# Kernel optimization log

Hardware: AMD Instinct MI355X
Metric: run time of the kernel (lower is better)

The kernel has to match this reference:

```python
import jax, jax.numpy as jnp
import numpy as np

HEADS = 8
DIM_HEAD = 64
QUERY_DIM = 512
CONTEXT_DIM = 512
OUT_DIM = 512
INNER = HEADS * DIM_HEAD  # 512


def setup_inputs() -> dict:
    key = jax.random.key(0)
    ks = jax.random.split(key, 6)
    B, N, S, M = 2, 1024, 4, 2048
    x = jax.random.normal(ks[0], (B, N, S, QUERY_DIM), dtype=jnp.float32)
    context = jax.random.normal(ks[1], (B, M, CONTEXT_DIM), dtype=jnp.float32)
    # Linear weights stored as [in, out] so y = x @ W (matches torch Linear with W.T)
    Wq = jax.random.normal(ks[2], (QUERY_DIM, INNER), dtype=jnp.float32) / np.sqrt(QUERY_DIM)
    Wkv = jax.random.normal(ks[3], (CONTEXT_DIM, 2 * INNER), dtype=jnp.float32) / np.sqrt(CONTEXT_DIM)
    Wo = jax.random.normal(ks[4], (INNER, OUT_DIM), dtype=jnp.float32) / np.sqrt(INNER)
    bo = jax.random.normal(ks[5], (OUT_DIM,), dtype=jnp.float32) * 0.01
    return {"x": x, "context": context, "Wq": Wq, "Wkv": Wkv, "Wo": Wo, "bo": bo}


def reference(x, context, Wq, Wkv, Wo, bo):
    B, N, S, _ = x.shape
    M = context.shape[1]
    scale = DIM_HEAD ** -0.5
    # projections
    q = (x @ Wq).reshape(B, N, S, HEADS, DIM_HEAD)            # b n s h d
    kv = context @ Wkv                                        # b m (2*inner)
    k, v = jnp.split(kv, 2, axis=-1)
    k = k.reshape(B, M, HEADS, DIM_HEAD)                      # b m h d
    v = v.reshape(B, M, HEADS, DIM_HEAD)
    # attention scores: [(b h) s n m] expressed as bhsnm
    sim = jnp.einsum('bnshd,bmhd->bhsnm', q, k) * scale
    attn = jax.nn.softmax(sim, axis=-1)
    out = jnp.einsum('bhsnm,bmhd->bnshd', attn, v)            # b n s h d
    out = out.reshape(B, N, S, INNER)
    return out @ Wo + bo
```

## Files before the change

### kernel.cpp

```cpp
#include <hip/hip_runtime.h>

typedef __bf16 bf16;
typedef __bf16 bf16x8 __attribute__((ext_vector_type(8)));
typedef __bf16 bf16x4 __attribute__((ext_vector_type(4)));
typedef float f32x4 __attribute__((ext_vector_type(4)));

#define SCL 0.18033688011112042f

#define GLOAD_LDS16(g, l)                                          \
  __builtin_amdgcn_global_load_lds(                                \
      (const __attribute__((address_space(1))) void*)(g),          \
      (__attribute__((address_space(3))) void*)(l), 16, 0, 0)

static __device__ __forceinline__ unsigned pk_bf16(float a, float b) {
  union { bf16 h[2]; unsigned u; } cv;
  cv.h[0] = (bf16)a; cv.h[1] = (bf16)b;
  return cv.u;
}
static __device__ __forceinline__ void pl32swap(unsigned& a, unsigned& b) {
  auto r = __builtin_amdgcn_permlane32_swap(a, b, false, false);
  a = r[0]; b = r[1];
}
static __device__ __forceinline__ void pl16swap(unsigned& a, unsigned& b) {
  auto r = __builtin_amdgcn_permlane16_swap(a, b, false, false);
  a = r[0]; b = r[1];
}

__global__ __launch_bounds__(256) void prep_kernel(const float* __restrict__ x,
                                                   const float* __restrict__ ctx,
                                                   const float* __restrict__ Wq,
                                                   const float* __restrict__ Wkv,
                                                   const float* __restrict__ Wo,
                                                   bf16* __restrict__ xb,
                                                   bf16* __restrict__ cb,
                                                   bf16* __restrict__ Wqt,
                                                   bf16* __restrict__ Wkvt,
                                                   bf16* __restrict__ Wot) {
  const int bid = blockIdx.x;
  const int tid = threadIdx.x;
  if (bid < 3072) {
    const float* src;
    bf16* dst;
    size_t off;
    if (bid < 2048) { src = x; dst = xb; off = (size_t)bid * 2048; }
    else            { src = ctx; dst = cb; off = (size_t)(bid - 2048) * 2048; }
    size_t i = off + (size_t)tid * 8;
    float4 a0 = *(const float4*)&src[i];
    float4 a1 = *(const float4*)&src[i + 4];
    bf16x8 o;
    o[0] = (bf16)a0.x; o[1] = (bf16)a0.y; o[2] = (bf16)a0.z; o[3] = (bf16)a0.w;
    o[4] = (bf16)a1.x; o[5] = (bf16)a1.y; o[6] = (bf16)a1.z; o[7] = (bf16)a1.w;
    *(bf16x8*)&dst[i] = o;
  } else {
    __shared__ float tile[32][33];
    const int idx = bid - 3072;
    const int bx = idx & 63;
    const int k0 = (idx >> 6) * 32;
    const float* W; bf16* Wt; int N, n0;
    if (bx < 16)      { W = Wq;  Wt = Wqt;  N = 512;  n0 = bx * 32; }
    else if (bx < 48) { W = Wkv; Wt = Wkvt; N = 1024; n0 = (bx - 16) * 32; }
    else              { W = Wo;  Wt = Wot;  N = 512;  n0 = (bx - 48) * 32; }
    const int j = tid & 31, i0 = tid >> 5;
#pragma unroll
    for (int ii = 0; ii < 4; ii++) {
      int i = i0 * 4 + ii;
      tile[i][j] = W[(size_t)(k0 + i) * N + n0 + j];
    }
    __syncthreads();
#pragma unroll
    for (int ii = 0; ii < 4; ii++) {
      int i = i0 * 4 + ii;
      Wt[(size_t)(n0 + i) * 512 + k0 + j] = (bf16)tile[j][i];
    }
  }
}

__device__ __forceinline__ void gemm128x64_core(const bf16* __restrict__ A,
                                                const bf16* __restrict__ Bt,
                                                int m0, int n0,
                                                bf16* As, bf16* Bs,
                                                f32x4 (&acc)[4][2],
                                                int wave, int lane) {
  const int l15 = lane & 15, quad = lane >> 4;
  const int psw = l15 & 7;
  const int lrow = lane >> 3;
  const int gchunk = (lane & 7) ^ lrow;
  const bf16* Ag = A + (size_t)(m0 + wave * 32 + lrow) * 512 + gchunk * 8;
  const bf16* Bg = Bt + (size_t)(n0 + wave * 16 + lrow) * 512 + gchunk * 8;
  bf16* Asw = As + wave * 32 * 64;
  bf16* Bsw = Bs + wave * 16 * 64;
  const int wm = (wave >> 1) * 64, wn = (wave & 1) * 32;

#pragma unroll
  for (int g = 0; g < 4; g++)
    GLOAD_LDS16(Ag + (size_t)(g * 8) * 512, Asw + g * 8 * 64);
#pragma unroll
  for (int g = 0; g < 2; g++)
    GLOAD_LDS16(Bg + (size_t)(g * 8) * 512, Bsw + g * 8 * 64);
  __syncthreads();

  for (int t = 0; t < 8; t++) {
    if (t < 7) {
      const int kt = (t + 1) * 64;
      const int nb = (t + 1) & 1;
#pragma unroll
      for (int g = 0; g < 4; g++)
        GLOAD_LDS16(Ag + kt + (size_t)(g * 8) * 512, Asw + nb * (128 * 64) + g * 8 * 64);
#pragma unroll
      for (int g = 0; g < 2; g++)
        GLOAD_LDS16(Bg + kt + (size_t)(g * 8) * 512, Bsw + nb * (64 * 64) + g * 8 * 64);
    }
    const bf16* Ac = As + (t & 1) * (128 * 64);
    const bf16* Bc = Bs + (t & 1) * (64 * 64);
#pragma unroll
    for (int h = 0; h < 2; h++) {
      bf16x8 af[4], bfr[2];
#pragma unroll
      for (int i = 0; i < 4; i++)
        af[i] = *(const bf16x8*)&Ac[(wm + i * 16 + l15) * 64 + (((h * 4 + quad) ^ psw) * 8)];
#pragma unroll
      for (int j = 0; j < 2; j++)
        bfr[j] = *(const bf16x8*)&Bc[(wn + j * 16 + l15) * 64 + (((h * 4 + quad) ^ psw) * 8)];
#pragma unroll
      for (int i = 0; i < 4; i++)
#pragma unroll
        for (int j = 0; j < 2; j++)
          acc[i][j] = __builtin_amdgcn_mfma_f32_16x16x32_bf16(af[i], bfr[j], acc[i][j], 0, 0, 0);
    }
    __syncthreads();
  }
}

__global__ __launch_bounds__(256, 2) void proj_kernel(const bf16* __restrict__ xb,
                                                      const bf16* __restrict__ cb,
                                                      const bf16* __restrict__ Wqt,
                                                      const bf16* __restrict__ Wkvt,
                                                      bf16* __restrict__ qb,
                                                      bf16* __restrict__ Kb,
                                                      bf16* __restrict__ Vtb) {
  __shared__ __align__(16) bf16 As[2 * 128 * 64];
  __shared__ __align__(16) bf16 Bs[2 * 64 * 64];
  const int tid = threadIdx.x;
  const int wave = tid >> 6, lane = tid & 63;
  const int quad = lane >> 4, l15 = lane & 15;
  const int bid = blockIdx.x;
  f32x4 acc[4][2] = {};
  const int wm = (wave >> 1) * 64, wn = (wave & 1) * 32;

  if (bid < 512) {
    const int m0 = (bid & 63) * 128, n0 = (bid >> 6) * 64;
    gemm128x64_core(xb, Wqt, m0, n0, As, Bs, acc, wave, lane);
#pragma unroll
    for (int i = 0; i < 4; i++) {
      const int rowb = m0 + wm + i * 16 + quad * 4;
#pragma unroll
      for (int j = 0; j < 2; j++) {
        const int col = n0 + wn + j * 16 + l15;
#pragma unroll
        for (int r = 0; r < 4; r++)
          qb[(size_t)(rowb + r) * 512 + col] = (bf16)(acc[i][j][r] * SCL);
      }
    }
  } else {
    const int idx = bid - 512;
    const int m0 = (idx & 31) * 128, n0 = (idx >> 5) * 64;
    gemm128x64_core(cb, Wkvt, m0, n0, As, Bs, acc, wave, lane);
#pragma unroll
    for (int i = 0; i < 4; i++) {
      const int rowb = m0 + wm + i * 16 + quad * 4;
#pragma unroll
      for (int j = 0; j < 2; j++) {
        const int col = n0 + wn + j * 16 + l15;
        if (col < 512) {
#pragma unroll
          for (int r = 0; r < 4; r++)
            Kb[(size_t)(rowb + r) * 512 + col] = (bf16)acc[i][j][r];
        } else {
          const int hh = (col - 512) >> 6, d = (col - 512) & 63;
          const int bb = rowb >> 11, mb = rowb & 2047;
          bf16x4 pk;
          pk[0] = (bf16)acc[i][j][0]; pk[1] = (bf16)acc[i][j][1];
          pk[2] = (bf16)acc[i][j][2]; pk[3] = (bf16)acc[i][j][3];
          *(bf16x4*)&Vtb[((size_t)(bb * 8 + hh) * 64 + d) * 2048 + mb] = pk;
        }
      }
    }
  }
}

__global__ __launch_bounds__(256, 2) void outproj_kernel(const bf16* __restrict__ attn,
                                                         const bf16* __restrict__ Wot,
                                                         float* __restrict__ out,
                                                         const float* __restrict__ bias) {
  __shared__ __align__(16) bf16 As[2 * 128 * 64];
  __shared__ __align__(16) bf16 Bs[2 * 64 * 64];
  const int tid = threadIdx.x;
  const int wave = tid >> 6, lane = tid & 63;
  const int quad = lane >> 4, l15 = lane & 15;
  const int bid = blockIdx.x;
  const int m0 = (bid & 63) * 128, n0 = (bid >> 6) * 64;
  f32x4 acc[4][2] = {};
  gemm128x64_core(attn, Wot, m0, n0, As, Bs, acc, wave, lane);
  const int wm = (wave >> 1) * 64, wn = (wave & 1) * 32;
#pragma unroll
  for (int i = 0; i < 4; i++) {
    const int rowb = m0 + wm + i * 16 + quad * 4;
#pragma unroll
    for (int j = 0; j < 2; j++) {
      const int col = n0 + wn + j * 16 + l15;
      const float bv = bias[col];
#pragma unroll
      for (int r = 0; r < 4; r++)
        out[(size_t)(rowb + r) * 512 + col] = acc[i][j][r] + bv;
    }
  }
}

__global__ __launch_bounds__(256, 2) void attn_kernel(const bf16* __restrict__ q,
                                                      const bf16* __restrict__ Kb,
                                                      const bf16* __restrict__ Vtb,
                                                      bf16* __restrict__ attn_out) {
  const int tid = threadIdx.x;
  const int wave = tid >> 6, lane = tid & 63;
  const int quad = lane >> 4, l15 = lane & 15;
  const int bid = blockIdx.x;
  const int g = bid & 15, inner = bid >> 4;
  const int b = g >> 3, h = g & 7;
  const int s = inner & 3, nt = inner >> 2;
  const int n0 = nt * 128;

  __shared__ __align__(16) bf16 Kl[2][64 * 64];
  __shared__ __align__(16) bf16 Vl[2][64 * 64];

  size_t qoff[2];
  bf16x8 qf[2][2];
#pragma unroll
  for (int cg = 0; cg < 2; cg++) {
    const int n = n0 + wave * 32 + cg * 16 + l15;
    qoff[cg] = ((size_t)((b * 1024 + n) * 4 + s)) * 512 + h * 64;
    qf[cg][0] = *(const bf16x8*)&q[qoff[cg] + quad * 8];
    qf[cg][1] = *(const bf16x8*)&q[qoff[cg] + 32 + quad * 8];
  }

  f32x4 o[2][4] = {};
  f32x4 ol[2] = {};
  bf16x8 ones;
#pragma unroll
  for (int i = 0; i < 8; i++) ones[i] = (bf16)1.0f;

  const int srow = tid >> 2, c0 = tid & 3;
  const bf16* Kg = Kb + (size_t)(b * 2048 + srow) * 512 + h * 64 + c0 * 16;
  const bf16* Vg = Vtb + ((size_t)(b * 8 + h) * 64 + srow) * 2048 + c0 * 16;
  const int ssw = srow & 7;
  const int koff0 = srow * 64 + ((c0 * 2) ^ ssw) * 8;
  const int koff1 = srow * 64 + ((c0 * 2 + 1) ^ ssw) * 8;

  uint4 kr0 = *(const uint4*)Kg;
  uint4 kr1 = *(const uint4*)(Kg + 8);
  uint4 vr0 = *(const uint4*)Vg;
  uint4 vr1 = *(const uint4*)(Vg + 8);
  *(uint4*)&Kl[0][koff0] = kr0; *(uint4*)&Kl[0][koff1] = kr1;
  *(uint4*)&Vl[0][koff0] = vr0; *(uint4*)&Vl[0][koff1] = vr1;

  const int psw = l15 & 7;

  for (int t = 0; t < 32; ++t) {
    __syncthreads();
    if (t < 31) {
      const bf16* kg = Kg + (size_t)(t + 1) * 64 * 512;
      const bf16* vg = Vg + (t + 1) * 64;
      kr0 = *(const uint4*)kg; kr1 = *(const uint4*)(kg + 8);
      vr0 = *(const uint4*)vg; vr1 = *(const uint4*)(vg + 8);
    }
    const bf16* Kc = &Kl[t & 1][0];
    const bf16* Vc = &Vl[t & 1][0];

    __builtin_amdgcn_s_setprio(1);

    f32x4 sf[2][4];
#pragma unroll
    for (int mc = 0; mc < 4; mc++) {
      bf16x8 kf0 = *(const bf16x8*)&Kc[(mc * 16 + l15) * 64 + ((quad ^ psw) * 8)];
      bf16x8 kf1 = *(const bf16x8*)&Kc[(mc * 16 + l15) * 64 + (((4 + quad) ^ psw) * 8)];
#pragma unroll
      for (int cg = 0; cg < 2; cg++) {
        f32x4 z = {};
        z = __builtin_amdgcn_mfma_f32_16x16x32_bf16(kf0, qf[cg][0], z, 0, 0, 0);
        z = __builtin_amdgcn_mfma_f32_16x16x32_bf16(kf1, qf[cg][1], z, 0, 0, 0);
        sf[cg][mc] = z;
      }
    }

    unsigned w[2][4][2];
#pragma unroll
    for (int cg = 0; cg < 2; cg++)
#pragma unroll
      for (int mc = 0; mc < 4; mc++) {
        const float e0 = __builtin_amdgcn_exp2f(sf[cg][mc][0]);
        const float e1 = __builtin_amdgcn_exp2f(sf[cg][mc][1]);
        const float e2 = __builtin_amdgcn_exp2f(sf[cg][mc][2]);
        const float e3 = __builtin_amdgcn_exp2f(sf[cg][mc][3]);
        w[cg][mc][0] = pk_bf16(e0, e1);
        w[cg][mc][1] = pk_bf16(e2, e3);
      }

    bf16x8 pf[2][2];
#pragma unroll
    for (int cg = 0; cg < 2; cg++)
#pragma unroll
      for (int mch = 0; mch < 2; mch++) {
        unsigned tw0, tw1, tw2, tw3;
        {
          unsigned a = w[cg][2 * mch][0], bb2 = w[cg][2 * mch + 1][0];
          pl32swap(a, bb2);
          pl16swap(a, bb2);
          tw0 = a; tw2 = bb2;
        }
        {
          unsigned a = w[cg][2 * mch][1], bb2 = w[cg][2 * mch + 1][1];
          pl32swap(a, bb2);
          pl16swap(a, bb2);
          tw1 = a; tw3 = bb2;
        }
        union { unsigned u[4]; bf16x8 v; } cv;
        cv.u[0] = tw0; cv.u[1] = tw1; cv.u[2] = tw2; cv.u[3] = tw3;
        pf[mch][cg] = cv.v;
      }

#pragma unroll
    for (int mch = 0; mch < 2; mch++) {
#pragma unroll
      for (int dg = 0; dg < 4; dg++) {
        bf16x8 vf = *(const bf16x8*)&Vc[(dg * 16 + l15) * 64 + (((mch * 4 + quad) ^ psw)) * 8];
#pragma unroll
        for (int cg = 0; cg < 2; cg++)
          o[cg][dg] = __builtin_amdgcn_mfma_f32_16x16x32_bf16(vf, pf[mch][cg], o[cg][dg], 0, 0, 0);
      }
#pragma unroll
      for (int cg = 0; cg < 2; cg++)
        ol[cg] = __builtin_amdgcn_mfma_f32_16x16x32_bf16(ones, pf[mch][cg], ol[cg], 0, 0, 0);
    }

    __builtin_amdgcn_s_setprio(0);

    if (t < 31) {
      bf16* Kn = &Kl[(t + 1) & 1][0];
      bf16* Vn = &Vl[(t + 1) & 1][0];
      *(uint4*)&Kn[koff0] = kr0; *(uint4*)&Kn[koff1] = kr1;
      *(uint4*)&Vn[koff0] = vr0; *(uint4*)&Vn[koff1] = vr1;
    }
  }

#pragma unroll
  for (int cg = 0; cg < 2; cg++) {
    const float inv = 1.0f / ol[cg][0];
#pragma unroll
    for (int dg = 0; dg < 4; dg++) {
      bf16x4 ok;
      ok[0] = (bf16)(o[cg][dg][0] * inv); ok[1] = (bf16)(o[cg][dg][1] * inv);
      ok[2] = (bf16)(o[cg][dg][2] * inv); ok[3] = (bf16)(o[cg][dg][3] * inv);
      *(bf16x4*)&attn_out[qoff[cg] + dg * 16 + quad * 4] = ok;
    }
  }
}

extern "C" void kernel_launch(void* const* d_in, const int* in_sizes, int n_in,
                              void* d_out, int out_size, void* d_ws, size_t ws_size,
                              hipStream_t stream) {
  const float* x = (const float*)d_in[0];
  const float* context = (const float*)d_in[1];
  const float* Wq = (const float*)d_in[2];
  const float* Wkv = (const float*)d_in[3];
  const float* Wo = (const float*)d_in[4];
  const float* bo = (const float*)d_in[5];
  float* out = (float*)d_out;

  char* ws = (char*)d_ws;
  bf16* xb   = (bf16*)(ws);
  bf16* cb   = (bf16*)(ws + (8u << 20));
  bf16* qb   = (bf16*)(ws + (12u << 20));
  bf16* Kb   = (bf16*)(ws + (20u << 20));
  bf16* Vtb  = (bf16*)(ws + (24u << 20));
  bf16* Wqt  = (bf16*)(ws + (28u << 20));
  bf16* Wkvt = (bf16*)(ws + (28u << 20) + 524288);
  bf16* Wot  = (bf16*)(ws + (28u << 20) + 1572864);
  bf16* attn = xb;

  prep_kernel<<<4096, 256, 0, stream>>>(x, context, Wq, Wkv, Wo, xb, cb, Wqt, Wkvt, Wot);
  proj_kernel<<<1024, 256, 0, stream>>>(xb, cb, Wqt, Wkvt, qb, Kb, Vtb);
  attn_kernel<<<512, 256, 0, stream>>>(qb, Kb, Vtb, attn);
  outproj_kernel<<<512, 256, 0, stream>>>(attn, Wot, out, bo);
}
```

Before: 151.3 us.

## Software-pipeline attention loop so QK of next tile overlaps PV of current

Restructures the flash-attention main loop into a skewed pipeline. Each iteration issues the QK^T MFMAs for tile t+1, then the PV MFMAs for tile t, then the exp/permute for t+1, with double-buffered P fragments. K is prefetched two tiles ahead and V one tile ahead. The aim is to hide the exp and permlane latency behind MFMA work, at the cost of more registers and more complex buffer indexing.

```diff
diff --git a/kernel.cpp b/kernel.cpp
--- a/kernel.cpp
+++ b/kernel.cpp
@@ -255,29 +255,13 @@
   const int koff0 = srow * 64 + ((c0 * 2) ^ ssw) * 8;
   const int koff1 = srow * 64 + ((c0 * 2 + 1) ^ ssw) * 8;
 
-  uint4 kr0 = *(const uint4*)Kg;
-  uint4 kr1 = *(const uint4*)(Kg + 8);
-  uint4 vr0 = *(const uint4*)Vg;
-  uint4 vr1 = *(const uint4*)(Vg + 8);
-  *(uint4*)&Kl[0][koff0] = kr0; *(uint4*)&Kl[0][koff1] = kr1;
-  *(uint4*)&Vl[0][koff0] = vr0; *(uint4*)&Vl[0][koff1] = vr1;
-
   const int psw = l15 & 7;
 
-  for (int t = 0; t < 32; ++t) {
-    __syncthreads();
-    if (t < 31) {
-      const bf16* kg = Kg + (size_t)(t + 1) * 64 * 512;
-      const bf16* vg = Vg + (t + 1) * 64;
-      kr0 = *(const uint4*)kg; kr1 = *(const uint4*)(kg + 8);
-      vr0 = *(const uint4*)vg; vr1 = *(const uint4*)(vg + 8);
-    }
-    const bf16* Kc = &Kl[t & 1][0];
-    const bf16* Vc = &Vl[t & 1][0];
-
-    __builtin_amdgcn_s_setprio(1);
-
-    f32x4 sf[2][4];
+  f32x4 sf[2][4];
+  bf16x8 pf_a[2][2], pf_b[2][2];
+  uint4 kr0, kr1, vr0, vr1;
+
+  auto qk_mfma = [&](const bf16* Kc) {
 #pragma unroll
     for (int mc = 0; mc < 4; mc++) {
       bf16x8 kf0 = *(const bf16x8*)&Kc[(mc * 16 + l15) * 64 + ((quad ^ psw) * 8)];
@@ -290,7 +274,9 @@
         sf[cg][mc] = z;
       }
     }
-
+  };
+
+  auto qk_finish = [&](bf16x8 (&pf)[2][2]) {
     unsigned w[2][4][2];
 #pragma unroll
     for (int cg = 0; cg < 2; cg++)
@@ -303,8 +289,6 @@
         w[cg][mc][0] = pk_bf16(e0, e1);
         w[cg][mc][1] = pk_bf16(e2, e3);
       }
-
-    bf16x8 pf[2][2];
 #pragma unroll
     for (int cg = 0; cg < 2; cg++)
 #pragma unroll
@@ -326,7 +310,9 @@
         cv.u[0] = tw0; cv.u[1] = tw1; cv.u[2] = tw2; cv.u[3] = tw3;
         pf[mch][cg] = cv.v;
       }
-
+  };
+
+  auto pv_step = [&](const bf16* Vc, const bf16x8 (&pf)[2][2]) {
 #pragma unroll
     for (int mch = 0; mch < 2; mch++) {
 #pragma unroll
@@ -340,15 +326,51 @@
       for (int cg = 0; cg < 2; cg++)
         ol[cg] = __builtin_amdgcn_mfma_f32_16x16x32_bf16(ones, pf[mch][cg], ol[cg], 0, 0, 0);
     }
-
+  };
+
+  kr0 = *(const uint4*)Kg;            kr1 = *(const uint4*)(Kg + 8);
+  vr0 = *(const uint4*)Vg;            vr1 = *(const uint4*)(Vg + 8);
+  *(uint4*)&Kl[0][koff0] = kr0; *(uint4*)&Kl[0][koff1] = kr1;
+  *(uint4*)&Vl[0][koff0] = vr0; *(uint4*)&Vl[0][koff1] = vr1;
+  kr0 = *(const uint4*)(Kg + 64 * 512);
+  kr1 = *(const uint4*)(Kg + 64 * 512 + 8);
+  __syncthreads();
+  qk_mfma(&Kl[0][0]);
+  *(uint4*)&Kl[1][koff0] = kr0; *(uint4*)&Kl[1][koff1] = kr1;
+  kr0 = *(const uint4*)(Kg + 2 * 64 * 512);
+  kr1 = *(const uint4*)(Kg + 2 * 64 * 512 + 8);
+  vr0 = *(const uint4*)(Vg + 64);
+  vr1 = *(const uint4*)(Vg + 64 + 8);
+  qk_finish(pf_a);
+
+  auto body = [&](int t, const bf16x8 (&pfc)[2][2], bf16x8 (&pfn)[2][2]) {
+    __syncthreads();
+    if (t < 30) {
+      bf16* Kn = &Kl[t & 1][0];
+      *(uint4*)&Kn[koff0] = kr0; *(uint4*)&Kn[koff1] = kr1;
+    }
+    if (t < 31) {
+      bf16* Vn = &Vl[(t + 1) & 1][0];
+      *(uint4*)&Vn[koff0] = vr0; *(uint4*)&Vn[koff1] = vr1;
+    }
+    if (t < 29) {
+      const bf16* kg = Kg + (size_t)(t + 3) * (64 * 512);
+      kr0 = *(const uint4*)kg; kr1 = *(const uint4*)(kg + 8);
+    }
+    if (t < 30) {
+      const bf16* vg = Vg + (size_t)(t + 2) * 64;
+      vr0 = *(const uint4*)vg; vr1 = *(const uint4*)(vg + 8);
+    }
+    __builtin_amdgcn_s_setprio(1);
+    if (t < 31) qk_mfma(&Kl[(t + 1) & 1][0]);
+    pv_step(&Vl[t & 1][0], pfc);
+    if (t < 31) qk_finish(pfn);
     __builtin_amdgcn_s_setprio(0);
-
-    if (t < 31) {
-      bf16* Kn = &Kl[(t + 1) & 1][0];
-      bf16* Vn = &Vl[(t + 1) & 1][0];
-      *(uint4*)&Kn[koff0] = kr0; *(uint4*)&Kn[koff1] = kr1;
-      *(uint4*)&Vn[koff0] = vr0; *(uint4*)&Vn[koff1] = vr1;
-    }
+  };
+
+  for (int tt = 0; tt < 16; ++tt) {
+    body(2 * tt, pf_a, pf_b);
+    body(2 * tt + 1, pf_b, pf_a);
   }
 
 #pragma unroll
```

Result: no change. 153.4 us (+1.3%).

## Fuse fp32-to-bf16 activation conversion into projection GEMM A-tile loads

Applied to the files above, without the earlier changes.

Drops the separate conversion pass that turned x and context into bf16 buffers. The projection GEMM now loads fp32 A tiles into registers, converts them to bf16 and writes them into swizzled LDS, with register prefetch of the next tile overlapping the MFMA work. This removes one full read and write of the activations through memory. The cost is twice the global A bytes per GEMM tile and extra register pressure and conversion instructions inside the main loop.

```diff
diff --git a/kernel.cpp b/kernel.cpp
--- a/kernel.cpp
+++ b/kernel.cpp
@@ -26,52 +26,32 @@
   a = r[0]; b = r[1];
 }
 
-__global__ __launch_bounds__(256) void prep_kernel(const float* __restrict__ x,
-                                                   const float* __restrict__ ctx,
-                                                   const float* __restrict__ Wq,
+__global__ __launch_bounds__(256) void prep_kernel(const float* __restrict__ Wq,
                                                    const float* __restrict__ Wkv,
                                                    const float* __restrict__ Wo,
-                                                   bf16* __restrict__ xb,
-                                                   bf16* __restrict__ cb,
                                                    bf16* __restrict__ Wqt,
                                                    bf16* __restrict__ Wkvt,
                                                    bf16* __restrict__ Wot) {
-  const int bid = blockIdx.x;
+  __shared__ float tile[32][33];
   const int tid = threadIdx.x;
-  if (bid < 3072) {
-    const float* src;
-    bf16* dst;
-    size_t off;
-    if (bid < 2048) { src = x; dst = xb; off = (size_t)bid * 2048; }
-    else            { src = ctx; dst = cb; off = (size_t)(bid - 2048) * 2048; }
-    size_t i = off + (size_t)tid * 8;
-    float4 a0 = *(const float4*)&src[i];
-    float4 a1 = *(const float4*)&src[i + 4];
-    bf16x8 o;
-    o[0] = (bf16)a0.x; o[1] = (bf16)a0.y; o[2] = (bf16)a0.z; o[3] = (bf16)a0.w;
-    o[4] = (bf16)a1.x; o[5] = (bf16)a1.y; o[6] = (bf16)a1.z; o[7] = (bf16)a1.w;
-    *(bf16x8*)&dst[i] = o;
-  } else {
-    __shared__ float tile[32][33];
-    const int idx = bid - 3072;
-    const int bx = idx & 63;
-    const int k0 = (idx >> 6) * 32;
-    const float* W; bf16* Wt; int N, n0;
-    if (bx < 16)      { W = Wq;  Wt = Wqt;  N = 512;  n0 = bx * 32; }
-    else if (bx < 48) { W = Wkv; Wt = Wkvt; N = 1024; n0 = (bx - 16) * 32; }
-    else              { W = Wo;  Wt = Wot;  N = 512;  n0 = (bx - 48) * 32; }
-    const int j = tid & 31, i0 = tid >> 5;
-#pragma unroll
-    for (int ii = 0; ii < 4; ii++) {
-      int i = i0 * 4 + ii;
-      tile[i][j] = W[(size_t)(k0 + i) * N + n0 + j];
-    }
-    __syncthreads();
-#pragma unroll
-    for (int ii = 0; ii < 4; ii++) {
-      int i = i0 * 4 + ii;
-      Wt[(size_t)(n0 + i) * 512 + k0 + j] = (bf16)tile[j][i];
-    }
+  const int idx = blockIdx.x;
+  const int bx = idx & 63;
+  const int k0 = (idx >> 6) * 32;
+  const float* W; bf16* Wt; int N, n0;
+  if (bx < 16)      { W = Wq;  Wt = Wqt;  N = 512;  n0 = bx * 32; }
+  else if (bx < 48) { W = Wkv; Wt = Wkvt; N = 1024; n0 = (bx - 16) * 32; }
+  else              { W = Wo;  Wt = Wot;  N = 512;  n0 = (bx - 48) * 32; }
+  const int j = tid & 31, i0 = tid >> 5;
+#pragma unroll
+  for (int ii = 0; ii < 4; ii++) {
+    int i = i0 * 4 + ii;
+    tile[i][j] = W[(size_t)(k0 + i) * N + n0 + j];
+  }
+  __syncthreads();
+#pragma unroll
+  for (int ii = 0; ii < 4; ii++) {
+    int i = i0 * 4 + ii;
+    Wt[(size_t)(n0 + i) * 512 + k0 + j] = (bf16)tile[j][i];
   }
 }
 
@@ -131,8 +111,85 @@
   }
 }
 
-__global__ __launch_bounds__(256, 2) void proj_kernel(const bf16* __restrict__ xb,
-                                                      const bf16* __restrict__ cb,
+__device__ __forceinline__ void gemm128x64_f32A_core(const float* __restrict__ A,
+                                                     const bf16* __restrict__ Bt,
+                                                     int m0, int n0,
+                                                     bf16* As, bf16* Bs,
+                                                     f32x4 (&acc)[4][2],
+                                                     int wave, int lane, int tid) {
+  const int l15 = lane & 15, quad = lane >> 4;
+  const int psw = l15 & 7;
+  const int lrow = lane >> 3;
+  const int gchunk = (lane & 7) ^ lrow;
+  const bf16* Bg = Bt + (size_t)(n0 + wave * 16 + lrow) * 512 + gchunk * 8;
+  bf16* Bsw = Bs + wave * 16 * 64;
+  const int arow0 = tid >> 4;
+  const int ac4 = tid & 15;
+  const int achunk = ac4 >> 1, ahalf = ac4 & 1;
+  const float* Ag = A + (size_t)(m0 + arow0) * 512 + ac4 * 4;
+  const int aoff0 = arow0 * 64 + ((achunk ^ (arow0 & 7)) * 8) + ahalf * 4;
+  const int wm = (wave >> 1) * 64, wn = (wave & 1) * 32;
+
+  float4 ar[8];
+#pragma unroll
+  for (int k = 0; k < 8; k++)
+    ar[k] = *(const float4*)(Ag + (size_t)(k * 16) * 512);
+#pragma unroll
+  for (int g = 0; g < 2; g++)
+    GLOAD_LDS16(Bg + (size_t)(g * 8) * 512, Bsw + g * 8 * 64);
+#pragma unroll
+  for (int k = 0; k < 8; k++) {
+    bf16x4 c;
+    c[0] = (bf16)ar[k].x; c[1] = (bf16)ar[k].y;
+    c[2] = (bf16)ar[k].z; c[3] = (bf16)ar[k].w;
+    *(bf16x4*)&As[aoff0 + k * 16 * 64] = c;
+  }
+  __syncthreads();
+
+  for (int t = 0; t < 8; t++) {
+    if (t < 7) {
+      const int kt = (t + 1) * 64;
+#pragma unroll
+      for (int k = 0; k < 8; k++)
+        ar[k] = *(const float4*)(Ag + kt + (size_t)(k * 16) * 512);
+      const int nb = (t + 1) & 1;
+#pragma unroll
+      for (int g = 0; g < 2; g++)
+        GLOAD_LDS16(Bg + kt + (size_t)(g * 8) * 512, Bs + nb * (64 * 64) + wave * 16 * 64 + g * 8 * 64);
+    }
+    const bf16* Ac = As + (t & 1) * (128 * 64);
+    const bf16* Bc = Bs + (t & 1) * (64 * 64);
+#pragma unroll
+    for (int h = 0; h < 2; h++) {
+      bf16x8 af[4], bfr[2];
+#pragma unroll
+      for (int i = 0; i < 4; i++)
+        af[i] = *(const bf16x8*)&Ac[(wm + i * 16 + l15) * 64 + (((h * 4 + quad) ^ psw) * 8)];
+#pragma unroll
+      for (int j = 0; j < 2; j++)
+        bfr[j] = *(const bf16x8*)&Bc[(wn + j * 16 + l15) * 64 + (((h * 4 + quad) ^ psw) * 8)];
+#pragma unroll
+      for (int i = 0; i < 4; i++)
+#pragma unroll
+        for (int j = 0; j < 2; j++)
+          acc[i][j] = __builtin_amdgcn_mfma_f32_16x16x32_bf16(af[i], bfr[j], acc[i][j], 0, 0, 0);
+    }
+    if (t < 7) {
+      bf16* And = As + ((t + 1) & 1) * (128 * 64);
+#pragma unroll
+      for (int k = 0; k < 8; k++) {
+        bf16x4 c;
+        c[0] = (bf16)ar[k].x; c[1] = (bf16)ar[k].y;
+        c[2] = (bf16)ar[k].z; c[3] = (bf16)ar[k].w;
+        *(bf16x4*)&And[aoff0 + k * 16 * 64] = c;
+      }
+    }
+    __syncthreads();
+  }
+}
+
+__global__ __launch_bounds__(256, 2) void proj_kernel(const float* __restrict__ x,
+                                                      const float* __restrict__ ctx,
                                                       const bf16* __restrict__ Wqt,
                                                       const bf16* __restrict__ Wkvt,
                                                       bf16* __restrict__ qb,
@@ -149,7 +206,7 @@
 
   if (bid < 512) {
     const int m0 = (bid & 63) * 128, n0 = (bid >> 6) * 64;
-    gemm128x64_core(xb, Wqt, m0, n0, As, Bs, acc, wave, lane);
+    gemm128x64_f32A_core(x, Wqt, m0, n0, As, Bs, acc, wave, lane, tid);
 #pragma unroll
     for (int i = 0; i < 4; i++) {
       const int rowb = m0 + wm + i * 16 + quad * 4;
@@ -164,7 +221,7 @@
   } else {
     const int idx = bid - 512;
     const int m0 = (idx & 31) * 128, n0 = (idx >> 5) * 64;
-    gemm128x64_core(cb, Wkvt, m0, n0, As, Bs, acc, wave, lane);
+    gemm128x64_f32A_core(ctx, Wkvt, m0, n0, As, Bs, acc, wave, lane, tid);
 #pragma unroll
     for (int i = 0; i < 4; i++) {
       const int rowb = m0 + wm + i * 16 + quad * 4;
@@ -376,18 +433,16 @@
   float* out = (float*)d_out;
 
   char* ws = (char*)d_ws;
-  bf16* xb   = (bf16*)(ws);
-  bf16* cb   = (bf16*)(ws + (8u << 20));
+  bf16* attn = (bf16*)(ws);
   bf16* qb   = (bf16*)(ws + (12u << 20));
   bf16* Kb   = (bf16*)(ws + (20u << 20));
   bf16* Vtb  = (bf16*)(ws + (24u << 20));
   bf16* Wqt  = (bf16*)(ws + (28u << 20));
   bf16* Wkvt = (bf16*)(ws + (28u << 20) + 524288);
   bf16* Wot  = (bf16*)(ws + (28u << 20) + 1572864);
-  bf16* attn = xb;
-
-  prep_kernel<<<4096, 256, 0, stream>>>(x, context, Wq, Wkv, Wo, xb, cb, Wqt, Wkvt, Wot);
-  proj_kernel<<<1024, 256, 0, stream>>>(xb, cb, Wqt, Wkvt, qb, Kb, Vtb);
+
+  prep_kernel<<<1024, 256, 0, stream>>>(Wq, Wkv, Wo, Wqt, Wkvt, Wot);
+  proj_kernel<<<1024, 256, 0, stream>>>(x, context, Wqt, Wkvt, qb, Kb, Vtb);
   attn_kernel<<<512, 256, 0, stream>>>(qb, Kb, Vtb, attn);
   outproj_kernel<<<512, 256, 0, stream>>>(attn, Wot, out, bo);
 }
```

After: 154.9 us. 2.3% more time.

## Split attention KV loop into two halves with a separate combine kernel

Applied to the files above, without the earlier changes.

Adds a split-K mode to the attention kernel. Each query tile is processed by two blocks, each covering half of the 2048 keys. Each block writes its unnormalized bf16 partial output and its softmax denominator, and a new combine kernel sums the two halves and normalizes. The goal is more parallelism and shorter per-block loops, at the cost of an extra launch, extra global traffic for the partial buffers, and an extra bf16 rounding of the partial sums. The mode is only enabled when the workspace is at least 35 MB; otherwise the old path runs.

```diff
diff --git a/kernel.cpp b/kernel.cpp
--- a/kernel.cpp
+++ b/kernel.cpp
@@ -219,14 +219,20 @@
 __global__ __launch_bounds__(256, 2) void attn_kernel(const bf16* __restrict__ q,
                                                       const bf16* __restrict__ Kb,
                                                       const bf16* __restrict__ Vtb,
-                                                      bf16* __restrict__ attn_out) {
+                                                      bf16* __restrict__ O1,
+                                                      bf16* __restrict__ O2,
+                                                      float* __restrict__ Lbuf,
+                                                      int splitk) {
   const int tid = threadIdx.x;
   const int wave = tid >> 6, lane = tid & 63;
   const int quad = lane >> 4, l15 = lane & 15;
   const int bid = blockIdx.x;
   const int g = bid & 15, inner = bid >> 4;
   const int b = g >> 3, h = g & 7;
-  const int s = inner & 3, nt = inner >> 2;
+  const int s = inner & 3;
+  int nt, half, t0, NT;
+  if (splitk) { nt = (inner >> 2) & 7; half = inner >> 5; t0 = half * 16; NT = 16; }
+  else        { nt = inner >> 2;       half = 0;          t0 = 0;         NT = 32; }
   const int n0 = nt * 128;
 
   __shared__ __align__(16) bf16 Kl[2][64 * 64];
@@ -255,25 +261,25 @@
   const int koff0 = srow * 64 + ((c0 * 2) ^ ssw) * 8;
   const int koff1 = srow * 64 + ((c0 * 2 + 1) ^ ssw) * 8;
 
-  uint4 kr0 = *(const uint4*)Kg;
-  uint4 kr1 = *(const uint4*)(Kg + 8);
-  uint4 vr0 = *(const uint4*)Vg;
-  uint4 vr1 = *(const uint4*)(Vg + 8);
+  uint4 kr0 = *(const uint4*)(Kg + (size_t)t0 * 64 * 512);
+  uint4 kr1 = *(const uint4*)(Kg + (size_t)t0 * 64 * 512 + 8);
+  uint4 vr0 = *(const uint4*)(Vg + t0 * 64);
+  uint4 vr1 = *(const uint4*)(Vg + t0 * 64 + 8);
   *(uint4*)&Kl[0][koff0] = kr0; *(uint4*)&Kl[0][koff1] = kr1;
   *(uint4*)&Vl[0][koff0] = vr0; *(uint4*)&Vl[0][koff1] = vr1;
 
   const int psw = l15 & 7;
 
-  for (int t = 0; t < 32; ++t) {
+  for (int tt = 0; tt < NT; ++tt) {
     __syncthreads();
-    if (t < 31) {
-      const bf16* kg = Kg + (size_t)(t + 1) * 64 * 512;
-      const bf16* vg = Vg + (t + 1) * 64;
+    if (tt < NT - 1) {
+      const bf16* kg = Kg + (size_t)(t0 + tt + 1) * 64 * 512;
+      const bf16* vg = Vg + (size_t)(t0 + tt + 1) * 64;
       kr0 = *(const uint4*)kg; kr1 = *(const uint4*)(kg + 8);
       vr0 = *(const uint4*)vg; vr1 = *(const uint4*)(vg + 8);
     }
-    const bf16* Kc = &Kl[t & 1][0];
-    const bf16* Vc = &Vl[t & 1][0];
+    const bf16* Kc = &Kl[tt & 1][0];
+    const bf16* Vc = &Vl[tt & 1][0];
 
     __builtin_amdgcn_s_setprio(1);
 
@@ -343,25 +349,60 @@
 
     __builtin_amdgcn_s_setprio(0);
 
-    if (t < 31) {
-      bf16* Kn = &Kl[(t + 1) & 1][0];
-      bf16* Vn = &Vl[(t + 1) & 1][0];
+    if (tt < NT - 1) {
+      bf16* Kn = &Kl[(tt + 1) & 1][0];
+      bf16* Vn = &Vl[(tt + 1) & 1][0];
       *(uint4*)&Kn[koff0] = kr0; *(uint4*)&Kn[koff1] = kr1;
       *(uint4*)&Vn[koff0] = vr0; *(uint4*)&Vn[koff1] = vr1;
     }
   }
 
-#pragma unroll
-  for (int cg = 0; cg < 2; cg++) {
-    const float inv = 1.0f / ol[cg][0];
-#pragma unroll
-    for (int dg = 0; dg < 4; dg++) {
-      bf16x4 ok;
-      ok[0] = (bf16)(o[cg][dg][0] * inv); ok[1] = (bf16)(o[cg][dg][1] * inv);
-      ok[2] = (bf16)(o[cg][dg][2] * inv); ok[3] = (bf16)(o[cg][dg][3] * inv);
-      *(bf16x4*)&attn_out[qoff[cg] + dg * 16 + quad * 4] = ok;
-    }
-  }
+  if (splitk) {
+    bf16* Op = half ? O2 : O1;
+#pragma unroll
+    for (int cg = 0; cg < 2; cg++) {
+#pragma unroll
+      for (int dg = 0; dg < 4; dg++) {
+        bf16x4 ok;
+        ok[0] = (bf16)o[cg][dg][0]; ok[1] = (bf16)o[cg][dg][1];
+        ok[2] = (bf16)o[cg][dg][2]; ok[3] = (bf16)o[cg][dg][3];
+        *(bf16x4*)&Op[qoff[cg] + dg * 16 + quad * 4] = ok;
+      }
+      if (quad == 0) {
+        const int m = (int)(qoff[cg] >> 9);
+        Lbuf[half * 65536 + m * 8 + h] = ol[cg][0];
+      }
+    }
+  } else {
+#pragma unroll
+    for (int cg = 0; cg < 2; cg++) {
+      const float inv = 1.0f / ol[cg][0];
+#pragma unroll
+      for (int dg = 0; dg < 4; dg++) {
+        bf16x4 ok;
+        ok[0] = (bf16)(o[cg][dg][0] * inv); ok[1] = (bf16)(o[cg][dg][1] * inv);
+        ok[2] = (bf16)(o[cg][dg][2] * inv); ok[3] = (bf16)(o[cg][dg][3] * inv);
+        *(bf16x4*)&O1[qoff[cg] + dg * 16 + quad * 4] = ok;
+      }
+    }
+  }
+}
+
+__global__ __launch_bounds__(256) void combine_kernel(bf16* __restrict__ O1,
+                                                      const bf16* __restrict__ O2,
+                                                      const float* __restrict__ Lbuf) {
+  const int i = blockIdx.x * 256 + threadIdx.x;
+  const int m = i >> 6, h = (i & 63) >> 3;
+  const float l1 = Lbuf[m * 8 + h];
+  const float l2 = Lbuf[65536 + m * 8 + h];
+  const float inv = 1.0f / (l1 + l2);
+  bf16x8 a = *(const bf16x8*)&O1[(size_t)i * 8];
+  bf16x8 c = *(const bf16x8*)&O2[(size_t)i * 8];
+  bf16x8 r;
+#pragma unroll
+  for (int j = 0; j < 8; j++)
+    r[j] = (bf16)(((float)a[j] + (float)c[j]) * inv);
+  *(bf16x8*)&O1[(size_t)i * 8] = r;
 }
 
 extern "C" void kernel_launch(void* const* d_in, const int* in_sizes, int n_in,
@@ -376,18 +417,43 @@
   float* out = (float*)d_out;
 
   char* ws = (char*)d_ws;
-  bf16* xb   = (bf16*)(ws);
-  bf16* cb   = (bf16*)(ws + (8u << 20));
-  bf16* qb   = (bf16*)(ws + (12u << 20));
-  bf16* Kb   = (bf16*)(ws + (20u << 20));
-  bf16* Vtb  = (bf16*)(ws + (24u << 20));
-  bf16* Wqt  = (bf16*)(ws + (28u << 20));
-  bf16* Wkvt = (bf16*)(ws + (28u << 20) + 524288);
-  bf16* Wot  = (bf16*)(ws + (28u << 20) + 1572864);
-  bf16* attn = xb;
+  const bool splitk = ws_size >= (35u << 20);
+
+  bf16 *qb, *Kb, *Vtb, *xb, *cb, *O1, *O2, *Wqt, *Wkvt, *Wot;
+  float* Lbuf;
+  if (splitk) {
+    qb   = (bf16*)(ws);
+    Kb   = (bf16*)(ws + (8u << 20));
+    Vtb  = (bf16*)(ws + (12u << 20));
+    xb   = (bf16*)(ws + (16u << 20));
+    cb   = (bf16*)(ws + (24u << 20));
+    O1   = xb;
+    O2   = (bf16*)(ws + (24u << 20));
+    Wqt  = (bf16*)(ws + (32u << 20));
+    Wkvt = (bf16*)(ws + (32u << 20) + 524288);
+    Wot  = (bf16*)(ws + (32u << 20) + 1572864);
+    Lbuf = (float*)(ws + (34u << 20));
+  } else {
+    xb   = (bf16*)(ws);
+    cb   = (bf16*)(ws + (8u << 20));
+    qb   = (bf16*)(ws + (12u << 20));
+    Kb   = (bf16*)(ws + (20u << 20));
+    Vtb  = (bf16*)(ws + (24u << 20));
+    Wqt  = (bf16*)(ws + (28u << 20));
+    Wkvt = (bf16*)(ws + (28u << 20) + 524288);
+    Wot  = (bf16*)(ws + (28u << 20) + 1572864);
+    O1   = xb;
+    O2   = xb;
+    Lbuf = (float*)Wqt;
+  }
 
   prep_kernel<<<4096, 256, 0, stream>>>(x, context, Wq, Wkv, Wo, xb, cb, Wqt, Wkvt, Wot);
   proj_kernel<<<1024, 256, 0, stream>>>(xb, cb, Wqt, Wkvt, qb, Kb, Vtb);
-  attn_kernel<<<512, 256, 0, stream>>>(qb, Kb, Vtb, attn);
-  outproj_kernel<<<512, 256, 0, stream>>>(attn, Wot, out, bo);
-}
+  if (splitk) {
+    attn_kernel<<<1024, 256, 0, stream>>>(qb, Kb, Vtb, O1, O2, Lbuf, 1);
+    combine_kernel<<<2048, 256, 0, stream>>>(O1, O2, Lbuf);
+  } else {
+    attn_kernel<<<512, 256, 0, stream>>>(qb, Kb, Vtb, O1, O2, Lbuf, 0);
+  }
+  outproj_kernel<<<512, 256, 0, stream>>>(O1, Wot, out, bo);
+}
```

Result: slower. 159.7 us (+5.5%).
